# Optimization experiments

Measured on AMD Instinct MI355X. Metric: run time of the kernel, lower is better.

The kernel has to match this reference:

```python
import math
import jax, jax.numpy as jnp
import numpy as np

N_HEADS = 16


def setup_inputs() -> dict:
    key = jax.random.key(0)
    k1, k2 = jax.random.split(key)
    N, H, C, T = 2, N_HEADS, 64, 2048
    qkv = jax.random.normal(k1, (N, H * 3 * C, T), dtype=jnp.float32)
    mask = jax.random.randint(k2, (N, 1, T), 0, 2).astype(bool) | (jnp.arange(T)[None, None, :] < T // 2)
    return {"qkv": qkv, "mask": mask}


def reference(qkv, mask):
    bs, width, length = qkv.shape
    ch = width // (3 * N_HEADS)
    qkv_r = qkv.reshape(bs * N_HEADS, 3 * ch, length)
    q, k, v = qkv_r[:, :ch], qkv_r[:, ch:2 * ch], qkv_r[:, 2 * ch:]
    scale = 1.0 / math.sqrt(math.sqrt(ch))
    # [bH, T, T] scores in float32 (matches weight.float())
    weight = jnp.einsum('bct,bcs->bts', q * scale, k * scale).astype(jnp.float32)
    inv = ~mask[:, 0, :]                                   # [N, T] True = pad
    m = inv[:, None, :] | inv[:, :, None]                  # [N, T, T]
    m = jnp.broadcast_to(m[:, None], (bs, N_HEADS, length, length)).reshape(-1, length, length)
    weight = jnp.where(m, jnp.finfo(weight.dtype).min, weight)
    weight = jax.nn.softmax(weight, axis=-1)
    a = jnp.einsum('bts,bcs->bct', weight, v)              # [bH, C, T]
    return a.reshape(bs, -1, length)
```

## Files before the change

### kernel.cpp

```cpp
#include <hip/hip_runtime.h>
#include <hip/hip_bf16.h>
#include <stdint.h>

namespace {

constexpr int T_LEN = 2048;
constexpr int NROWS = 192;
constexpr int QBLK  = 64;
constexpr int NBH   = 32;
constexpr int KT_STRIDE = 72;
constexpr int TILE_ELEMS = 64 * KT_STRIDE;
constexpr int TILE_BYTES = TILE_ELEMS * 2;

typedef float f32x4 __attribute__((ext_vector_type(4)));
typedef short bf16x8 __attribute__((ext_vector_type(8)));
typedef short bf16x4 __attribute__((ext_vector_type(4)));

__device__ __forceinline__ unsigned short f2bf(float f) {
  union { float f; unsigned u; } v; v.f = f;
  unsigned r = v.u + 0x7fffu + ((v.u >> 16) & 1u);
  return (unsigned short)(r >> 16);
}
__device__ __forceinline__ unsigned pack2(float a, float b) {
  return (unsigned)f2bf(a) | ((unsigned)f2bf(b) << 16);
}
__device__ __forceinline__ float fast_exp2(float x) {
#if __has_builtin(__builtin_amdgcn_exp2f)
  return __builtin_amdgcn_exp2f(x);
#else
  return exp2f(x);
#endif
}
__device__ __forceinline__ f32x4 mfma_16x16x16_bf16(bf16x4 a, bf16x4 b, f32x4 c) {
#if __has_builtin(__builtin_amdgcn_mfma_f32_16x16x16bf16_1k)
  return __builtin_amdgcn_mfma_f32_16x16x16bf16_1k(a, b, c, 0, 0, 0);
#else
  asm("v_mfma_f32_16x16x16_bf16 %0, %1, %2, %0" : "+v"(c) : "v"(a), "v"(b));
  return c;
#endif
}
__device__ __forceinline__ void gload_lds16(const void* g, void* l) {
  __builtin_amdgcn_global_load_lds(
      (const __attribute__((address_space(1))) unsigned int*)g,
      (__attribute__((address_space(3))) unsigned int*)l, 16, 0, 0);
}

}

__global__ void nm_kernel(const unsigned char* __restrict__ raw,
                          unsigned char* __restrict__ outm, int n) {
  int stride = (raw[1] != 0) ? 1 : ((raw[4] != 0) ? 4 : 8);
  int i = blockIdx.x * blockDim.x + threadIdx.x;
  if (i < n) outm[i] = (raw[(size_t)i * stride] != 0) ? 1 : 0;
}

__global__ __launch_bounds__(256) void prep12_kernel(const float* __restrict__ qkv,
                                                     const unsigned char* __restrict__ mraw,
                                                     short* __restrict__ qtg,
                                                     short* __restrict__ ktg,
                                                     short* __restrict__ vtg,
                                                     float* __restrict__ bias,
                                                     int mask_elems) {
  const int z  = blockIdx.z;
  const int bh = blockIdx.y;
  const int bx = blockIdx.x;
  const int t  = threadIdx.x;

  if (z >= 2) {
    int cid = ((bh * 64) + (z - 2) * 32 + bx) * 256 + t;
    int bh2 = cid >> 14;
    int rem = cid & 16383;
    int c = rem >> 8;
    int cg = rem & 255;
    int grp = cg >> 3, jin = cg & 7;
    const float* src = qkv + (size_t)bh2 * NROWS * T_LEN + (size_t)(128 + c) * T_LEN + cg * 8;
    float4 a = *(const float4*)src;
    float4 b = *(const float4*)(src + 4);
    bf16x4 o0, o1;
    o0[0] = (short)f2bf(a.x); o0[1] = (short)f2bf(a.y);
    o0[2] = (short)f2bf(a.z); o0[3] = (short)f2bf(a.w);
    o1[0] = (short)f2bf(b.x); o1[1] = (short)f2bf(b.y);
    o1[2] = (short)f2bf(b.z); o1[3] = (short)f2bf(b.w);
    short* d = vtg + (size_t)(bh2 * 32 + grp) * TILE_ELEMS + c * KT_STRIDE + jin * 8;
    *(bf16x4*)d = o0;
    *(bf16x4*)(d + 4) = o1;
    if (z == 2 && bh == 0 && bx < 24) {
      int i = bx * 256 + t;
      int stride = (mraw[1] != 0) ? 1 : ((mraw[4] != 0) ? 4 : 8);
      if (i < mask_elems) bias[i] = (mraw[(size_t)i * stride] != 0) ? 0.0f : -1.0e30f;
      else if (i < mask_elems + T_LEN) bias[i] = 0.0f;
    }
    return;
  }

  __shared__ float tile[64][65];
  const int s0 = bx * 64;
  const float* src = qkv + (size_t)bh * NROWS * T_LEN + (size_t)z * 64 * T_LEN;
  const int c = t >> 2;
  #pragma unroll
  for (int p = 0; p < 4; ++p) {
    int col = (t & 3) * 4 + p * 16;
    float4 v = *(const float4*)&src[(size_t)c * T_LEN + s0 + col];
    tile[c][col] = v.x; tile[c][col + 1] = v.y;
    tile[c][col + 2] = v.z; tile[c][col + 3] = v.w;
  }
  __syncthreads();
  const int s = t & 63;
  float scale;
  if (z) {
    scale = 1.0f;
  } else {
    const int mstride = (mraw[1] != 0) ? 1 : ((mraw[4] != 0) ? 4 : 8);
    const int nb = bh >> 4;
    const bool live = mraw[((size_t)nb * T_LEN + s0 + s) * mstride] != 0;
    scale = live ? 0.18033688011112042f : 0.0f;
  }
  #pragma unroll
  for (int p = 0; p < 2; ++p) {
    int jc = (t >> 6) * 2 + p;
    bf16x4 o0, o1;
    #pragma unroll
    for (int i = 0; i < 4; ++i) {
      o0[i] = (short)f2bf(tile[jc * 8 + i][s] * scale);
      o1[i] = (short)f2bf(tile[jc * 8 + 4 + i][s] * scale);
    }
    short* d = z
      ? (ktg + (size_t)(bh * 32 + bx) * TILE_ELEMS + s * KT_STRIDE + jc * 8)
      : (qtg + (size_t)bh * T_LEN * 64 + (size_t)(s0 + s) * 64 + jc * 8);
    *(bf16x4*)d = o0;
    *(bf16x4*)(d + 4) = o1;
  }
}


__global__ __launch_bounds__(512, 4) void attn11_kernel(const short* __restrict__ qtg,
                                                        const short* __restrict__ ktg,
                                                        const short* __restrict__ vtg,
                                                        const float* __restrict__ bias,
                                                        int mask_elems,
                                                        float* __restrict__ out) {
  __shared__ __align__(16) short smem[4 * TILE_ELEMS];

  const int tid  = threadIdx.x;
  const int lane = tid & 63;
  const int wv   = tid >> 6;
  const int sgrp = wv & 3;
  const int tgrp = wv >> 2;
  const int l15  = lane & 15;
  const int g    = lane >> 4;

  int id = blockIdx.x;
  id = (id & 7) * 128 + (id >> 3);
  const int bh = id >> 5;
  const int t0 = (id & 31) * QBLK;
  const int nb = bh >> 4;

  const int tA = t0 + (tgrp * 2) * 16 + l15;
  const int tB = tA + 16;

  const short* Qbase = qtg + (size_t)bh * T_LEN * 64;
  const bf16x8 qfA0 = *(const bf16x8*)(Qbase + (size_t)tA * 64 + g * 8);
  const bf16x8 qfA1 = *(const bf16x8*)(Qbase + (size_t)tA * 64 + 32 + g * 8);
  const bf16x8 qfB0 = *(const bf16x8*)(Qbase + (size_t)tB * 64 + g * 8);
  const bf16x8 qfB1 = *(const bf16x8*)(Qbase + (size_t)tB * 64 + 32 + g * 8);

  const float btA = bias[(size_t)nb * T_LEN + tA];
  const float btB = bias[(size_t)nb * T_LEN + tB];
  const float* __restrict__ browA = bias + ((btA != 0.0f) ? (size_t)mask_elems
                                                          : (size_t)nb * T_LEN);
  const float* __restrict__ browB = bias + ((btB != 0.0f) ? (size_t)mask_elems
                                                          : (size_t)nb * T_LEN);

  const char* __restrict__ kt0 = (const char*)(ktg + (size_t)bh * 32 * TILE_ELEMS);
  const char* __restrict__ vt0 = (const char*)(vtg + (size_t)bh * 32 * TILE_ELEMS);
  char* KtL = (char*)smem;
  char* VsL = (char*)(smem + 2 * TILE_ELEMS);

  gload_lds16(kt0 + wv * 1024 + lane * 16, KtL + wv * 1024);
  gload_lds16(vt0 + wv * 1024 + lane * 16, VsL + wv * 1024);
  if (wv == 0) gload_lds16(kt0 + 8192 + lane * 16, KtL + 8192);
  if (wv == 1) gload_lds16(vt0 + 8192 + lane * 16, VsL + 8192);
  __syncthreads();

  f32x4 accA[4], accB[4];
  #pragma unroll
  for (int i = 0; i < 4; ++i) { accA[i] = (f32x4){0.f,0.f,0.f,0.f}; accB[i] = accA[i]; }
  float lA = 0.0f, lB = 0.0f;

  const int koff = (sgrp * 16 + l15) * KT_STRIDE;
  const int boff = sgrp * 16 + g * 4;

  int cur = 0;
  for (int sb = 0; sb < T_LEN / 64; ++sb) {
    if (sb + 1 < T_LEN / 64) {
      const char* ks = kt0 + (size_t)(sb + 1) * TILE_BYTES;
      const char* vs = vt0 + (size_t)(sb + 1) * TILE_BYTES;
      char* Ktn = KtL + (cur ^ 1) * TILE_BYTES;
      char* Vsn = VsL + (cur ^ 1) * TILE_BYTES;
      gload_lds16(ks + wv * 1024 + lane * 16, Ktn + wv * 1024);
      gload_lds16(vs + wv * 1024 + lane * 16, Vsn + wv * 1024);
      if (wv == 0) gload_lds16(ks + 8192 + lane * 16, Ktn + 8192);
      if (wv == 1) gload_lds16(vs + 8192 + lane * 16, Vsn + 8192);
    }

    const short* Ktc = smem + cur * TILE_ELEMS;
    const short* Vsc = smem + (2 + cur) * TILE_ELEMS;

    bf16x8 kf0 = *(const bf16x8*)&Ktc[koff + g * 8];
    bf16x8 kf1 = *(const bf16x8*)&Ktc[koff + 32 + g * 8];

    f32x4 SA = (f32x4){0.f, 0.f, 0.f, 0.f};
    SA = __builtin_amdgcn_mfma_f32_16x16x32_bf16(kf0, qfA0, SA, 0, 0, 0);
    SA = __builtin_amdgcn_mfma_f32_16x16x32_bf16(kf1, qfA1, SA, 0, 0, 0);
    f32x4 SB = (f32x4){0.f, 0.f, 0.f, 0.f};
    SB = __builtin_amdgcn_mfma_f32_16x16x32_bf16(kf0, qfB0, SB, 0, 0, 0);
    SB = __builtin_amdgcn_mfma_f32_16x16x32_bf16(kf1, qfB1, SB, 0, 0, 0);

    const f32x4 b4A = *(const f32x4*)&browA[sb * 64 + boff];
    const f32x4 b4B = *(const f32x4*)&browB[sb * 64 + boff];
    float pA0 = fast_exp2(SA[0] + b4A[0]);
    float pA1 = fast_exp2(SA[1] + b4A[1]);
    float pA2 = fast_exp2(SA[2] + b4A[2]);
    float pA3 = fast_exp2(SA[3] + b4A[3]);
    lA += (pA0 + pA1) + (pA2 + pA3);
    float pB0 = fast_exp2(SB[0] + b4B[0]);
    float pB1 = fast_exp2(SB[1] + b4B[1]);
    float pB2 = fast_exp2(SB[2] + b4B[2]);
    float pB3 = fast_exp2(SB[3] + b4B[3]);
    lB += (pB0 + pB1) + (pB2 + pB3);

    union { bf16x4 v; __hip_bfloat162 h[2]; } pfA, pfB;
    pfA.h[0] = __float22bfloat162_rn(float2{pA0, pA1});
    pfA.h[1] = __float22bfloat162_rn(float2{pA2, pA3});
    pfB.h[0] = __float22bfloat162_rn(float2{pB0, pB1});
    pfB.h[1] = __float22bfloat162_rn(float2{pB2, pB3});

    #pragma unroll
    for (int cb = 0; cb < 4; ++cb) {
      bf16x4 vf = *(const bf16x4*)&Vsc[(cb * 16 + l15) * KT_STRIDE + sgrp * 16 + g * 4];
      accA[cb] = mfma_16x16x16_bf16(vf, pfA.v, accA[cb]);
      accB[cb] = mfma_16x16x16_bf16(vf, pfB.v, accB[cb]);
    }

    __syncthreads();
    cur ^= 1;
  }

  float* scr = (float*)smem;
  {
    const int lb = lane * 36;
    if (sgrp >= 2) {
      float* base = scr + ((sgrp - 2) * 2 + tgrp) * 2304 + lb;
      #pragma unroll
      for (int cb = 0; cb < 4; ++cb) {
        *(f32x4*)&base[cb * 4] = accA[cb];
        *(f32x4*)&base[16 + cb * 4] = accB[cb];
      }
      base[32] = lA; base[33] = lB;
    }
    __syncthreads();
    if (sgrp < 2) {
      const float* base = scr + (sgrp * 2 + tgrp) * 2304 + lb;
      #pragma unroll
      for (int cb = 0; cb < 4; ++cb) {
        accA[cb] += *(const f32x4*)&base[cb * 4];
        accB[cb] += *(const f32x4*)&base[16 + cb * 4];
      }
      lA += base[32]; lB += base[33];
    }
    __syncthreads();
    if (sgrp == 1) {
      float* base = scr + tgrp * 2304 + lb;
      #pragma unroll
      for (int cb = 0; cb < 4; ++cb) {
        *(f32x4*)&base[cb * 4] = accA[cb];
        *(f32x4*)&base[16 + cb * 4] = accB[cb];
      }
      base[32] = lA; base[33] = lB;
    }
    __syncthreads();
    if (sgrp == 0) {
      const float* base = scr + tgrp * 2304 + lb;
      #pragma unroll
      for (int cb = 0; cb < 4; ++cb) {
        accA[cb] += *(const f32x4*)&base[cb * 4];
        accB[cb] += *(const f32x4*)&base[16 + cb * 4];
      }
      lA += base[32]; lB += base[33];

      lA += __shfl_xor(lA, 16, 64);
      lA += __shfl_xor(lA, 32, 64);
      lB += __shfl_xor(lB, 16, 64);
      lB += __shfl_xor(lB, 32, 64);
      const float ilA = 1.0f / lA;
      const float ilB = 1.0f / lB;
      const size_t out_base = (size_t)bh * 64 * T_LEN;
      #pragma unroll
      for (int cb = 0; cb < 4; ++cb) {
        #pragma unroll
        for (int r = 0; r < 4; ++r) {
          int c = cb * 16 + g * 4 + r;
          out[out_base + (size_t)c * T_LEN + tA] = accA[cb][r] * ilA;
          out[out_base + (size_t)c * T_LEN + tB] = accB[cb][r] * ilB;
        }
      }
    }
  }
}


__global__ __launch_bounds__(256) void attn_fb_kernel(const float* __restrict__ qkv,
                                                      const unsigned char* __restrict__ maskn,
                                                      float* __restrict__ out) {
  __shared__ __align__(16) short Kt[QBLK * KT_STRIDE];
  __shared__ __align__(16) short Vs[64 * KT_STRIDE];
  __shared__ __align__(16) unsigned char Ms[T_LEN];

  const int tid  = threadIdx.x;
  const int lane = tid & 63;
  const int wv   = tid >> 6;
  const int l15  = lane & 15;
  const int g    = lane >> 4;

  const int bh = blockIdx.y;
  const int nb = bh >> 4;
  const int t0 = blockIdx.x * QBLK;

  const float* __restrict__ Qg = qkv + (size_t)bh * NROWS * T_LEN;
  const float* __restrict__ Kg = Qg + (size_t)64 * T_LEN;
  const float* __restrict__ Vg = Qg + (size_t)128 * T_LEN;

  {
    const uint2* src = (const uint2*)(maskn + (size_t)nb * T_LEN);
    ((uint2*)Ms)[tid] = src[tid];
  }
  {
    const int c2 = (tid >> 6) * 2;
    const int s  = tid & 63;
    #pragma unroll
    for (int p = 0; p < 8; ++p) {
      int c = p * 8 + c2;
      float f0 = Qg[(size_t)c * T_LEN + t0 + s] * 0.125f;
      float f1 = Qg[(size_t)(c + 1) * T_LEN + t0 + s] * 0.125f;
      *(unsigned*)&Kt[s * KT_STRIDE + c] = pack2(f0, f1);
    }
  }
  __syncthreads();

  bf16x8 qf0 = *(const bf16x8*)&Kt[(wv * 16 + l15) * KT_STRIDE + g * 8];
  bf16x8 qf1 = *(const bf16x8*)&Kt[(wv * 16 + l15) * KT_STRIDE + 32 + g * 8];
  const int t_lane = t0 + wv * 16 + l15;
  const bool invt = (Ms[t_lane] == 0);

  f32x4 acc[4];
  #pragma unroll
  for (int i = 0; i < 4; ++i) acc[i] = (f32x4){0.f, 0.f, 0.f, 0.f};
  float m_run = -3.0e38f;
  float l_run = 0.0f;

  for (int sb = 0; sb < T_LEN / 64; ++sb) {
    const int s0 = sb * 64;
    __syncthreads();
    {
      const int c2 = (tid >> 6) * 2;
      const int s  = tid & 63;
      #pragma unroll
      for (int p = 0; p < 8; ++p) {
        int c = p * 8 + c2;
        float f0 = Kg[(size_t)c * T_LEN + s0 + s];
        float f1 = Kg[(size_t)(c + 1) * T_LEN + s0 + s];
        *(unsigned*)&Kt[s * KT_STRIDE + c] = pack2(f0, f1);
      }
    }
    {
      const int cv = (tid >> 5);
      const int s2 = tid & 31;
      #pragma unroll
      for (int p = 0; p < 8; ++p) {
        int c = p * 8 + cv;
        float2 f = *(const float2*)&Vg[(size_t)c * T_LEN + s0 + 2 * s2];
        *(unsigned*)&Vs[c * KT_STRIDE + 2 * s2] = pack2(f.x, f.y);
      }
    }
    __syncthreads();

    #pragma unroll
    for (int st = 0; st < 4; ++st) {
      const int srow = st * 16 + l15;
      bf16x8 kf0 = *(const bf16x8*)&Kt[srow * KT_STRIDE + g * 8];
      bf16x8 kf1 = *(const bf16x8*)&Kt[srow * KT_STRIDE + 32 + g * 8];
      f32x4 S = (f32x4){0.f, 0.f, 0.f, 0.f};
      S = __builtin_amdgcn_mfma_f32_16x16x32_bf16(kf0, qf0, S, 0, 0, 0);
      S = __builtin_amdgcn_mfma_f32_16x16x32_bf16(kf1, qf1, S, 0, 0, 0);

      const unsigned m4 = *(const unsigned*)&Ms[s0 + st * 16 + g * 4];
      float vals[4];
      #pragma unroll
      for (int r = 0; r < 4; ++r) {
        float x = ((m4 >> (8 * r)) & 0xffu) ? S[r] : -1.0e30f;
        vals[r] = invt ? 0.0f : x;
      }
      float pm = fmaxf(fmaxf(vals[0], vals[1]), fmaxf(vals[2], vals[3]));
      pm = fmaxf(pm, __shfl_xor(pm, 16, 64));
      pm = fmaxf(pm, __shfl_xor(pm, 32, 64));
      const float newm = fmaxf(m_run, pm);
      const float alpha = fast_exp2((m_run - newm) * 1.44269504f);
      float p0 = fast_exp2((vals[0] - newm) * 1.44269504f);
      float p1 = fast_exp2((vals[1] - newm) * 1.44269504f);
      float p2 = fast_exp2((vals[2] - newm) * 1.44269504f);
      float p3 = fast_exp2((vals[3] - newm) * 1.44269504f);
      float ps = (p0 + p1) + (p2 + p3);
      ps += __shfl_xor(ps, 16, 64);
      ps += __shfl_xor(ps, 32, 64);
      l_run = l_run * alpha + ps;
      m_run = newm;
      if (__any(alpha < 1.0f)) {
        #pragma unroll
        for (int cb = 0; cb < 4; ++cb)
          #pragma unroll
          for (int r = 0; r < 4; ++r) acc[cb][r] *= alpha;
      }
      bf16x4 pf;
      pf[0] = (short)f2bf(p0); pf[1] = (short)f2bf(p1);
      pf[2] = (short)f2bf(p2); pf[3] = (short)f2bf(p3);
      #pragma unroll
      for (int cb = 0; cb < 4; ++cb) {
        bf16x4 vf = *(const bf16x4*)&Vs[(cb * 16 + l15) * KT_STRIDE + st * 16 + g * 4];
        acc[cb] = mfma_16x16x16_bf16(vf, pf, acc[cb]);
      }
    }
  }

  const float il = 1.0f / l_run;
  const size_t out_base = (size_t)bh * 64 * T_LEN;
  #pragma unroll
  for (int cb = 0; cb < 4; ++cb) {
    #pragma unroll
    for (int r = 0; r < 4; ++r) {
      int c = cb * 16 + g * 4 + r;
      out[out_base + (size_t)c * T_LEN + t_lane] = acc[cb][r] * il;
    }
  }
}


extern "C" void kernel_launch(void* const* d_in, const int* in_sizes, int n_in,
                              void* d_out, int out_size, void* d_ws, size_t ws_size,
                              hipStream_t stream) {
  (void)n_in; (void)out_size;
  const float* qkv = (const float*)d_in[0];
  const unsigned char* mraw = (const unsigned char*)d_in[1];
  float* out = (float*)d_out;
  const int mask_elems = in_sizes[1];

  const size_t QSZ = (size_t)NBH * T_LEN * 64 * sizeof(short);
  const size_t TSZ = (size_t)NBH * 32 * TILE_ELEMS * sizeof(short);
  const size_t BSZ = (size_t)(mask_elems + T_LEN) * sizeof(float);
  const size_t need = QSZ + 2 * TSZ + BSZ;
  if (ws_size >= need) {
    short* qtg = (short*)d_ws;
    short* ktg = (short*)((char*)d_ws + QSZ);
    short* vtg = (short*)((char*)d_ws + QSZ + TSZ);
    float* bias = (float*)((char*)d_ws + QSZ + 2 * TSZ);
    prep12_kernel<<<dim3(32, NBH, 4), 256, 0, stream>>>(qkv, mraw, qtg, ktg, vtg,
                                                        bias, mask_elems);
    attn11_kernel<<<dim3(NBH * 32), 512, 0, stream>>>(qtg, ktg, vtg, bias,
                                                      mask_elems, out);
  } else {
    unsigned char* maskn = (unsigned char*)d_ws;
    nm_kernel<<<(mask_elems + 255) / 256, 256, 0, stream>>>(mraw, maskn, mask_elems);
    attn_fb_kernel<<<dim3(T_LEN / QBLK, NBH), 256, 0, stream>>>(qkv, maskn, out);
  }
}
```

Measured before the change: 84.98 us.

## Triple-buffer K/V tiles with fine-grained vmcnt waits and stage bias row in LDS

Replaces the double-buffered K/V LDS pipeline with a three-slot ring that prefetches two tiles ahead. The full __syncthreads at the end of each iteration becomes an explicit s_waitcnt vmcnt on only the older loads plus s_barrier, so global loads overlap more of the compute. The per-key bias row is now staged once per block in LDS as bf16 and applied through an fma with a per-row live flag, replacing per-iteration global loads that selected one of two bias rows. This raises LDS use (possibly lowering occupancy), rounds the bias to bf16, and depends on hand-counted vmcnt values being correct.

```diff
diff --git a/kernel.cpp b/kernel.cpp
--- a/kernel.cpp
+++ b/kernel.cpp
@@ -23,6 +23,11 @@
 }
 __device__ __forceinline__ unsigned pack2(float a, float b) {
   return (unsigned)f2bf(a) | ((unsigned)f2bf(b) << 16);
+}
+__device__ __forceinline__ float bf2f(short s) {
+  union { unsigned u; float f; } v;
+  v.u = ((unsigned)(unsigned short)s) << 16;
+  return v.f;
 }
 __device__ __forceinline__ float fast_exp2(float x) {
 #if __has_builtin(__builtin_amdgcn_exp2f)
@@ -133,13 +138,12 @@
 }
 
 
-__global__ __launch_bounds__(512, 4) void attn11_kernel(const short* __restrict__ qtg,
+__global__ __launch_bounds__(512, 4) void attn15_kernel(const short* __restrict__ qtg,
                                                         const short* __restrict__ ktg,
                                                         const short* __restrict__ vtg,
                                                         const float* __restrict__ bias,
-                                                        int mask_elems,
                                                         float* __restrict__ out) {
-  __shared__ __align__(16) short smem[4 * TILE_ELEMS];
+  __shared__ __align__(16) short smem[6 * TILE_ELEMS + T_LEN];
 
   const int tid  = threadIdx.x;
   const int lane = tid & 63;
@@ -155,7 +159,7 @@
   const int t0 = (id & 31) * QBLK;
   const int nb = bh >> 4;
 
-  const int tA = t0 + (tgrp * 2) * 16 + l15;
+  const int tA = t0 + tgrp * 32 + l15;
   const int tB = tA + 16;
 
   const short* Qbase = qtg + (size_t)bh * T_LEN * 64;
@@ -164,23 +168,40 @@
   const bf16x8 qfB0 = *(const bf16x8*)(Qbase + (size_t)tB * 64 + g * 8);
   const bf16x8 qfB1 = *(const bf16x8*)(Qbase + (size_t)tB * 64 + 32 + g * 8);
 
-  const float btA = bias[(size_t)nb * T_LEN + tA];
-  const float btB = bias[(size_t)nb * T_LEN + tB];
-  const float* __restrict__ browA = bias + ((btA != 0.0f) ? (size_t)mask_elems
-                                                          : (size_t)nb * T_LEN);
-  const float* __restrict__ browB = bias + ((btB != 0.0f) ? (size_t)mask_elems
-                                                          : (size_t)nb * T_LEN);
+  const float liveA = (bias[(size_t)nb * T_LEN + tA] == 0.0f) ? 1.0f : 0.0f;
+  const float liveB = (bias[(size_t)nb * T_LEN + tB] == 0.0f) ? 1.0f : 0.0f;
+
+  char* KtL = (char*)smem;
+  char* VsL = (char*)smem + 3 * TILE_BYTES;
+  short* biasL = smem + 6 * TILE_ELEMS;
+
+  {
+    f32x4 bv = *(const f32x4*)&bias[(size_t)nb * T_LEN + tid * 4];
+    union { bf16x4 v; __hip_bfloat162 h[2]; } bb;
+    bb.h[0] = __float22bfloat162_rn(float2{bv[0], bv[1]});
+    bb.h[1] = __float22bfloat162_rn(float2{bv[2], bv[3]});
+    *(bf16x4*)&biasL[tid * 4] = bb.v;
+  }
 
   const char* __restrict__ kt0 = (const char*)(ktg + (size_t)bh * 32 * TILE_ELEMS);
   const char* __restrict__ vt0 = (const char*)(vtg + (size_t)bh * 32 * TILE_ELEMS);
-  char* KtL = (char*)smem;
-  char* VsL = (char*)(smem + 2 * TILE_ELEMS);
-
-  gload_lds16(kt0 + wv * 1024 + lane * 16, KtL + wv * 1024);
-  gload_lds16(vt0 + wv * 1024 + lane * 16, VsL + wv * 1024);
-  if (wv == 0) gload_lds16(kt0 + 8192 + lane * 16, KtL + 8192);
-  if (wv == 1) gload_lds16(vt0 + 8192 + lane * 16, VsL + 8192);
-  __syncthreads();
+
+  auto ISSUE = [&](int j, int r) {
+    const char* ks = kt0 + (size_t)j * TILE_BYTES;
+    const char* vs = vt0 + (size_t)j * TILE_BYTES;
+    char* kd = KtL + r * TILE_BYTES;
+    char* vd = VsL + r * TILE_BYTES;
+    gload_lds16(ks + wv * 1024 + lane * 16, kd + wv * 1024);
+    gload_lds16(vs + wv * 1024 + lane * 16, vd + wv * 1024);
+    if (wv == 0) gload_lds16(ks + 8192 + lane * 16, kd + 8192);
+    if (wv == 1) gload_lds16(vs + 8192 + lane * 16, vd + 8192);
+  };
+
+  ISSUE(0, 0);
+  ISSUE(1, 1);
+  if (wv < 2) asm volatile("s_waitcnt vmcnt(3) lgkmcnt(0)" ::: "memory");
+  else        asm volatile("s_waitcnt vmcnt(2) lgkmcnt(0)" ::: "memory");
+  __builtin_amdgcn_s_barrier();
 
   f32x4 accA[4], accB[4];
   #pragma unroll
@@ -190,21 +211,15 @@
   const int koff = (sgrp * 16 + l15) * KT_STRIDE;
   const int boff = sgrp * 16 + g * 4;
 
-  int cur = 0;
+  int ring = 0;
   for (int sb = 0; sb < T_LEN / 64; ++sb) {
-    if (sb + 1 < T_LEN / 64) {
-      const char* ks = kt0 + (size_t)(sb + 1) * TILE_BYTES;
-      const char* vs = vt0 + (size_t)(sb + 1) * TILE_BYTES;
-      char* Ktn = KtL + (cur ^ 1) * TILE_BYTES;
-      char* Vsn = VsL + (cur ^ 1) * TILE_BYTES;
-      gload_lds16(ks + wv * 1024 + lane * 16, Ktn + wv * 1024);
-      gload_lds16(vs + wv * 1024 + lane * 16, Vsn + wv * 1024);
-      if (wv == 0) gload_lds16(ks + 8192 + lane * 16, Ktn + 8192);
-      if (wv == 1) gload_lds16(vs + 8192 + lane * 16, Vsn + 8192);
-    }
-
-    const short* Ktc = smem + cur * TILE_ELEMS;
-    const short* Vsc = smem + (2 + cur) * TILE_ELEMS;
+    if (sb + 2 < T_LEN / 64) {
+      int r2 = ring + 2; if (r2 >= 3) r2 -= 3;
+      ISSUE(sb + 2, r2);
+    }
+
+    const short* Ktc = (const short*)(KtL + ring * TILE_BYTES);
+    const short* Vsc = (const short*)(VsL + ring * TILE_BYTES);
 
     bf16x8 kf0 = *(const bf16x8*)&Ktc[koff + g * 8];
     bf16x8 kf1 = *(const bf16x8*)&Ktc[koff + 32 + g * 8];
@@ -216,17 +231,18 @@
     SB = __builtin_amdgcn_mfma_f32_16x16x32_bf16(kf0, qfB0, SB, 0, 0, 0);
     SB = __builtin_amdgcn_mfma_f32_16x16x32_bf16(kf1, qfB1, SB, 0, 0, 0);
 
-    const f32x4 b4A = *(const f32x4*)&browA[sb * 64 + boff];
-    const f32x4 b4B = *(const f32x4*)&browB[sb * 64 + boff];
-    float pA0 = fast_exp2(SA[0] + b4A[0]);
-    float pA1 = fast_exp2(SA[1] + b4A[1]);
-    float pA2 = fast_exp2(SA[2] + b4A[2]);
-    float pA3 = fast_exp2(SA[3] + b4A[3]);
+    const bf16x4 braw = *(const bf16x4*)&biasL[sb * 64 + boff];
+    const float b0 = bf2f(braw[0]), b1 = bf2f(braw[1]);
+    const float b2 = bf2f(braw[2]), b3 = bf2f(braw[3]);
+    float pA0 = fast_exp2(__builtin_fmaf(b0, liveA, SA[0]));
+    float pA1 = fast_exp2(__builtin_fmaf(b1, liveA, SA[1]));
+    float pA2 = fast_exp2(__builtin_fmaf(b2, liveA, SA[2]));
+    float pA3 = fast_exp2(__builtin_fmaf(b3, liveA, SA[3]));
     lA += (pA0 + pA1) + (pA2 + pA3);
-    float pB0 = fast_exp2(SB[0] + b4B[0]);
-    float pB1 = fast_exp2(SB[1] + b4B[1]);
-    float pB2 = fast_exp2(SB[2] + b4B[2]);
-    float pB3 = fast_exp2(SB[3] + b4B[3]);
+    float pB0 = fast_exp2(__builtin_fmaf(b0, liveB, SB[0]));
+    float pB1 = fast_exp2(__builtin_fmaf(b1, liveB, SB[1]));
+    float pB2 = fast_exp2(__builtin_fmaf(b2, liveB, SB[2]));
+    float pB3 = fast_exp2(__builtin_fmaf(b3, liveB, SB[3]));
     lB += (pB0 + pB1) + (pB2 + pB3);
 
     union { bf16x4 v; __hip_bfloat162 h[2]; } pfA, pfB;
@@ -242,8 +258,14 @@
       accB[cb] = mfma_16x16x16_bf16(vf, pfB.v, accB[cb]);
     }
 
-    __syncthreads();
-    cur ^= 1;
+    if (sb < T_LEN / 64 - 2) {
+      if (wv < 2) asm volatile("s_waitcnt vmcnt(3)" ::: "memory");
+      else        asm volatile("s_waitcnt vmcnt(2)" ::: "memory");
+    } else {
+      asm volatile("s_waitcnt vmcnt(0)" ::: "memory");
+    }
+    __builtin_amdgcn_s_barrier();
+    ring = (ring == 2) ? 0 : ring + 1;
   }
 
   float* scr = (float*)smem;
@@ -464,8 +486,7 @@
     float* bias = (float*)((char*)d_ws + QSZ + 2 * TSZ);
     prep12_kernel<<<dim3(32, NBH, 4), 256, 0, stream>>>(qkv, mraw, qtg, ktg, vtg,
                                                         bias, mask_elems);
-    attn11_kernel<<<dim3(NBH * 32), 512, 0, stream>>>(qtg, ktg, vtg, bias,
-                                                      mask_elems, out);
+    attn15_kernel<<<dim3(NBH * 32), 512, 0, stream>>>(qtg, ktg, vtg, bias, out);
   } else {
     unsigned char* maskn = (unsigned char*)d_ws;
     nm_kernel<<<(mask_elems + 255) / 256, 256, 0, stream>>>(mraw, maskn, mask_elems);
```

Result: faster. 79.79 us (-6.1%).
